# Kernel tuning notes

Hardware: AMD Instinct MI355X
Metric: run time of the kernel (lower is better)

## Reference

```python
import jax, jax.numpy as jnp
import numpy as np
from jax.scipy.special import logsumexp

TAG_NAMES = ['<pad>', 'O', 'B-PER', 'I-PER', 'B-LOC', 'I-LOC', 'B-ORG', 'I-ORG', 'B-MISC', 'I-MISC']
K = len(TAG_NAMES)
T, B, D = 512, 64, 1024
PAD = 0
IMP = -100.0
VOCAB = 30000


def _crf_params(rng):
    # torchcrf reset_parameters: uniform(-0.1, 0.1), then init_crf_transitions overrides
    start = rng.uniform(-0.1, 0.1, K).astype(np.float32)
    end = rng.uniform(-0.1, 0.1, K).astype(np.float32)
    trans = rng.uniform(-0.1, 0.1, (K, K)).astype(np.float32)
    for i, name in enumerate(TAG_NAMES):
        if name[0] in ('I', 'L') or name == '<pad>':
            start[i] = IMP
        if name[0] in ('B', 'I'):
            end[i] = IMP
    tag_is = {p: [i for i, t in enumerate(TAG_NAMES) if t[0] == p] for p in 'BIOUL'}
    tag_is['P'] = [i for i, t in enumerate(TAG_NAMES) if t == 'tag']
    for ft, tos in {'B': 'BOUP', 'I': 'BOUP', 'O': 'IL', 'U': 'IL'}.items():
        for fi in tag_is[ft]:
            for tt in tos:
                for ti in tag_is[tt]:
                    trans[fi, ti] = IMP
    for ft, tos in {'B': 'IL', 'I': 'IL'}.items():
        for fi in tag_is[ft]:
            for tt in tos:
                for ti in tag_is[tt]:
                    if TAG_NAMES[fi].split('-')[1] != TAG_NAMES[ti].split('-')[1]:
                        trans[fi, ti] = IMP
    return jnp.asarray(start), jnp.asarray(end), jnp.asarray(trans)


def setup_inputs() -> dict:
    rng = np.random.default_rng(0)
    # torchcrf requires mask[0] == 1 everywhere and contiguous masks -> build from lengths
    lengths = rng.integers(T // 2, T + 1, size=B)
    valid = np.arange(T)[:, None] < lengths[None, :]  # (T, B)
    words = np.where(valid, rng.integers(1, VOCAB, size=(T, B)), PAD).astype(np.int64)
    tags = rng.integers(0, K, size=(T, B)).astype(np.int64)
    word_features = rng.standard_normal((T, B, D)).astype(np.float32)
    W = (rng.standard_normal((D, K)) / np.sqrt(D)).astype(np.float32)
    b = np.zeros(K, np.float32)
    start, end, trans = _crf_params(rng)
    return dict(words=jnp.asarray(words), tags=jnp.asarray(tags),
                word_features=jnp.asarray(word_features), W=jnp.asarray(W), b=jnp.asarray(b),
                start_trans=start, end_trans=end, transitions=trans)


def _crf_loss(emissions, tags, maskf, start, end, trans):
    """-log p(tags | emissions), summed over batch (torchcrf reduction='sum')."""
    bidx = jnp.arange(emissions.shape[1])
    # gold-path score (numerator)
    score0 = start[tags[0]] + emissions[0, bidx, tags[0]]
    em_tag = jnp.take_along_axis(emissions[1:], tags[1:, :, None], axis=-1)[..., 0]  # (T-1,B)
    step = trans[tags[:-1], tags[1:]] + em_tag
    numer = score0 + jnp.sum(step * maskf[1:], axis=0)
    seq_ends = maskf.sum(0).astype(jnp.int32) - 1
    numer = numer + end[tags[seq_ends, bidx]]
    # partition function (forward algorithm, stable log-sum-exp scan)
    def fwd_step(score, xs):
        em_t, m_t = xs
        nxt = logsumexp(score[:, :, None] + trans[None] + em_t[:, None, :], axis=1)  # (B,K)
        return jnp.where(m_t[:, None] > 0, nxt, score), None
    score, _ = jax.lax.scan(fwd_step, start[None] + emissions[0], (emissions[1:], maskf[1:]))
    denom = logsumexp(score + end[None], axis=1)
    return -(numer - denom).sum()


def _crf_decode(emissions, maskf, start, end, trans):
    """Viterbi decode; returns (T,B) int32 paths, 0-padded past sequence ends."""
    bidx = jnp.arange(emissions.shape[1])
    def vit_step(score, xs):
        em_t, m_t = xs
        bcast = score[:, :, None] + trans[None] + em_t[:, None, :]  # (B, K_prev, K_cur)
        best = bcast.max(axis=1)
        idx = bcast.argmax(axis=1).astype(jnp.int32)
        return jnp.where(m_t[:, None] > 0, best, score), idx
    score, history = jax.lax.scan(vit_step, start[None] + emissions[0], (emissions[1:], maskf[1:]))
    last_tag = jnp.argmax(score + end[None], axis=1).astype(jnp.int32)  # tag at seq_end per batch
    def back_step(tag, xs):
        hist_t, m_t = xs
        prev = jnp.where(m_t > 0, hist_t[bidx, tag], tag)
        return prev, prev
    _, path_head = jax.lax.scan(back_step, last_tag, (history, maskf[1:]), reverse=True)
    paths = jnp.concatenate([path_head, last_tag[None]], axis=0)  # (T, B)
    return jnp.where(maskf > 0, paths, 0)


def reference(words, tags, word_features, W, b, start_trans, end_trans, transitions):
    # eval-mode dropout is identity; fc projects features to tag emissions
    emissions = word_features @ W + b  # (T, B, K)
    maskf = (words != PAD).astype(emissions.dtype)  # (T, B)
    paths = _crf_decode(emissions, maskf, start_trans, end_trans, transitions)
    loss = _crf_loss(emissions, tags, maskf, start_trans, end_trans, transitions)
    return paths, loss
```

## Files before the change

kernel.cpp:

```cpp
#include <hip/hip_runtime.h>
#include <hip/hip_bf16.h>

#define TT 512
#define BB 64
#define KK 10
#define DD 1024
#define CL 32
#define NC 16

typedef unsigned char uchar;
typedef short bf16x8 __attribute__((ext_vector_type(8)));
typedef float f32x4 __attribute__((ext_vector_type(4)));

__device__ __forceinline__ unsigned f2bf(float f) {
    unsigned u = __float_as_uint(f);
    return (u + 0x7FFFu + ((u >> 16) & 1u)) >> 16;
}

__device__ __forceinline__ float max10(const float* r) {
    float m0 = fmaxf(r[0], r[1]), m1 = fmaxf(r[2], r[3]);
    float m2 = fmaxf(r[4], r[5]), m3 = fmaxf(r[6], r[7]);
    float m4 = fmaxf(r[8], r[9]);
    m0 = fmaxf(m0, m1); m2 = fmaxf(m2, m3); m0 = fmaxf(m0, m2);
    return fmaxf(m0, m4);
}

__device__ __forceinline__ float lse10(const float* r) {
    const float m = max10(r);
    float s0 = __expf(r[0] - m) + __expf(r[1] - m);
    float s1 = __expf(r[2] - m) + __expf(r[3] - m);
    float s2 = __expf(r[4] - m) + __expf(r[5] - m);
    float s3 = __expf(r[6] - m) + __expf(r[7] - m);
    float s4 = __expf(r[8] - m) + __expf(r[9] - m);
    return m + __logf(((s0 + s1) + (s2 + s3)) + s4);
}

__global__ __launch_bounds__(512) void k_emissions(
    const int* __restrict__ words, const float* __restrict__ wf,
    const float* __restrict__ W, const float* __restrict__ bias,
    float* __restrict__ em, int* __restrict__ lenArr, float* loss_slot) {
    const int tid = threadIdx.x;
    if (blockIdx.x == 256) {
        __shared__ int cnt[8][64];
        const int b = tid & 63, seg = tid >> 6;
        int c = 0;
        for (int t = seg; t < TT; t += 8) c += (words[t * BB + b] != 0) ? 1 : 0;
        cnt[seg][b] = c;
        __syncthreads();
        if (tid < 64) {
            int s = 0;
            #pragma unroll
            for (int g = 0; g < 8; ++g) s += cnt[g][tid];
            lenArr[tid] = s;
        }
        if (tid == 0) *loss_slot = 0.f;
        return;
    }

    __shared__ uint4 Bfrag[32][64];
    for (int idx = tid; idx < 32 * 64; idx += 512) {
        const int ks = idx >> 6, l = idx & 63;
        const int col = l & 15, kg = l >> 4;
        unsigned u[4];
        #pragma unroll
        for (int p = 0; p < 4; ++p) {
            unsigned lo = 0, hi = 0;
            if (col < KK) {
                const int k0 = ks * 32 + kg * 8 + p * 2;
                lo = f2bf(W[(size_t)k0 * KK + col]);
                hi = f2bf(W[(size_t)(k0 + 1) * KK + col]);
            }
            u[p] = lo | (hi << 16);
        }
        Bfrag[ks][l] = make_uint4(u[0], u[1], u[2], u[3]);
    }
    __syncthreads();

    const int wave = tid >> 6, lane = tid & 63;
    const int arow = lane & 15;
    const int kg   = lane >> 4;
    const int row0 = blockIdx.x * 128 + wave * 16;
    const float* ap = wf + (size_t)(row0 + arow) * DD + kg * 8;
    const float bk = bias[arow < KK ? arow : 0];

    f32x4 acc = {0.f, 0.f, 0.f, 0.f};
    float4 fa[4], fb[4];
    #pragma unroll
    for (int p = 0; p < 4; ++p) {
        fa[p] = *reinterpret_cast<const float4*>(ap + p * 32);
        fb[p] = *reinterpret_cast<const float4*>(ap + p * 32 + 4);
    }
    uint4 bcur[8], bnxt[8];
    #pragma unroll
    for (int q = 0; q < 8; ++q) bcur[q] = Bfrag[q][lane];

    #pragma unroll
    for (int ph = 0; ph < 4; ++ph) {
        if (ph < 3) {
            #pragma unroll
            for (int q = 0; q < 8; ++q) bnxt[q] = Bfrag[(ph + 1) * 8 + q][lane];
        }
        #pragma unroll
        for (int q = 0; q < 8; ++q) {
            const int ks = ph * 8 + q;
            const int s = ks & 3;
            bf16x8 afr;
            afr[0] = (short)f2bf(fa[s].x); afr[1] = (short)f2bf(fa[s].y);
            afr[2] = (short)f2bf(fa[s].z); afr[3] = (short)f2bf(fa[s].w);
            afr[4] = (short)f2bf(fb[s].x); afr[5] = (short)f2bf(fb[s].y);
            afr[6] = (short)f2bf(fb[s].z); afr[7] = (short)f2bf(fb[s].w);
            if (ks < 28) {
                fa[s] = *reinterpret_cast<const float4*>(ap + (ks + 4) * 32);
                fb[s] = *reinterpret_cast<const float4*>(ap + (ks + 4) * 32 + 4);
            }
            union { uint4 u; bf16x8 v; } bu;
            bu.u = bcur[q];
            acc = __builtin_amdgcn_mfma_f32_16x16x32_bf16(afr, bu.v, acc, 0, 0, 0);
        }
        #pragma unroll
        for (int q = 0; q < 8; ++q) bcur[q] = bnxt[q];
    }
    if (arow < KK) {
        #pragma unroll
        for (int r = 0; r < 4; ++r)
            em[(size_t)(row0 + kg * 4 + r) * KK + arow] = acc[r] + bk;
    }
}

__global__ __launch_bounds__(128) void k_chunk(
    const float* __restrict__ em, const float* __restrict__ trans,
    const int* __restrict__ lenArr, float* __restrict__ Mlse, float* __restrict__ Mmax) {
    int id = blockIdx.x;
    const bool mx = id >= 1024; id &= 1023;
    const int b = id >> 4, c = id & 15;
    const int len = lenArr[b];
    const int s_lo = c * CL + 1;
    const int s_hi = min(c * CL + CL, len - 1);
    const int ns = s_hi - s_lo + 1;
    if (ns <= 0) return;

    __shared__ float Ms[KK][12];
    __shared__ float eml[CL][KK];
    const int tid = threadIdx.x;
    for (int idx = tid; idx < CL * KK; idx += 128) {
        const int sl = idx / KK, j = idx % KK;
        const int s = s_lo + sl;
        eml[sl][j] = (s <= TT - 1) ? em[((size_t)s * BB + b) * KK + j] : 0.f;
    }
    const int i = tid / KK, j = tid % KK;
    const bool act = tid < KK * KK;
    float trc[KK];
    if (act) {
        #pragma unroll
        for (int k = 0; k < KK; ++k) trc[k] = trans[k * KK + j];
    }
    __syncthreads();
    float cur = 0.f;
    if (act) { cur = trans[i * KK + j] + eml[0][j]; Ms[i][j] = cur; }
    __syncthreads();
    for (int sl = 1; sl < ns; ++sl) {
        float row[KK];
        if (act) {
            #pragma unroll
            for (int k = 0; k < KK; ++k) row[k] = Ms[i][k] + trc[k];
        }
        __syncthreads();
        if (act) {
            cur = (mx ? max10(row) : lse10(row)) + eml[sl][j];
            Ms[i][j] = cur;
        }
        __syncthreads();
    }
    if (act) {
        float* out = mx ? Mmax : Mlse;
        out[((size_t)b * NC + c) * 100 + i * KK + j] = cur;
    }
}

__global__ __launch_bounds__(1024) void k_crf(
    const int* __restrict__ tags, const float* __restrict__ em,
    const float* __restrict__ startv, const float* __restrict__ endv,
    const float* __restrict__ trans, const int* __restrict__ lenArr,
    const float* __restrict__ Mlse, const float* __restrict__ Mmax,
    int* __restrict__ paths, float* __restrict__ loss_slot) {
    const int b = blockIdx.x;
    const int tid = threadIdx.x;
    const int wv = tid >> 6, lane = tid & 63;
    const int len = lenArr[b];

    __shared__ float Ml[NC][100];
    __shared__ float Mm[NC][100];
    __shared__ float eml[NC][CL][KK];
    __shared__ float ub[NC][KK];
    __shared__ uchar hl[NC][CL * KK];
    __shared__ int   Fl[NC][KK];
    __shared__ int   vt[NC + 1];
    __shared__ float em0[KK];
    __shared__ float red[2];

    for (int idx = tid; idx < NC * 100; idx += 1024) {
        Ml[idx / 100][idx % 100] = Mlse[(size_t)b * NC * 100 + idx];
        Mm[idx / 100][idx % 100] = Mmax[(size_t)b * NC * 100 + idx];
    }
    for (int idx = tid; idx < NC * CL * KK; idx += 1024) {
        const int c = idx / (CL * KK), r = idx % (CL * KK);
        const int sl = r / KK, j = r % KK;
        const int s = c * CL + 1 + sl;
        eml[c][sl][j] = (s <= TT - 1) ? em[((size_t)s * BB + b) * KK + j] : 0.f;
    }
    if (tid < KK) em0[tid] = em[(size_t)b * KK + tid];
    __syncthreads();

    if (wv == 0) {
        float v[KK];
        #pragma unroll
        for (int i = 0; i < KK; ++i) v[i] = startv[i] + em0[i];
        for (int c = 0; c < NC; ++c) {
            if (lane < KK) ub[c][lane] = v[lane];
            const int s_hi = min(c * CL + CL, len - 1);
            if (s_hi >= c * CL + 1) {
                float nv = 0.f;
                if (lane < KK) {
                    float r[KK];
                    #pragma unroll
                    for (int k = 0; k < KK; ++k) r[k] = v[k] + Mm[c][k * KK + lane];
                    nv = max10(r);
                }
                #pragma unroll
                for (int i = 0; i < KK; ++i) v[i] = __shfl(nv, i);
            }
        }
        float best = v[0] + endv[0];
        int bi = 0;
        #pragma unroll
        for (int i = 1; i < KK; ++i) {
            const float x = v[i] + endv[i];
            if (x > best) { best = x; bi = i; }
        }
        if (lane == 0) vt[NC] = bi;
    } else if (wv == 1) {
        float v[KK];
        #pragma unroll
        for (int i = 0; i < KK; ++i) v[i] = startv[i] + em0[i];
        for (int c = 0; c < NC; ++c) {
            const int s_hi = min(c * CL + CL, len - 1);
            if (s_hi >= c * CL + 1) {
                float nv = 0.f;
                if (lane < KK) {
                    float r[KK];
                    #pragma unroll
                    for (int k = 0; k < KK; ++k) r[k] = v[k] + Ml[c][k * KK + lane];
                    nv = lse10(r);
                }
                #pragma unroll
                for (int i = 0; i < KK; ++i) v[i] = __shfl(nv, i);
            }
        }
        float r[KK];
        #pragma unroll
        for (int i = 0; i < KK; ++i) r[i] = v[i] + endv[i];
        if (lane == 0) red[0] = lse10(r);
    } else if (wv == 2) {
        float part = 0.f;
        for (int t = 1 + lane; t < len; t += 64) {
            const int tp = tags[(t - 1) * BB + b];
            const int tc = tags[t * BB + b];
            part += trans[tp * KK + tc] + eml[(t - 1) >> 5][(t - 1) & 31][tc];
        }
        #pragma unroll
        for (int off = 32; off >= 1; off >>= 1) part += __shfl_xor(part, off);
        if (lane == 0) {
            const int t0 = tags[b];
            const int te = tags[(len - 1) * BB + b];
            red[1] = part + startv[t0] + em0[t0] + endv[te];
        }
    }
    __syncthreads();

    {
        const int c = wv;
        const int s_hi = min(c * CL + CL, len - 1);
        const int ns = s_hi - (c * CL + 1) + 1;
        if (ns > 0) {
            float trc[KK];
            if (lane < KK) {
                #pragma unroll
                for (int i = 0; i < KK; ++i) trc[i] = trans[i * KK + lane];
            }
            float s[KK];
            #pragma unroll
            for (int i = 0; i < KK; ++i) s[i] = ub[c][i];
            for (int sl = 0; sl < ns; ++sl) {
                float best = s[0] + trc[0];
                int bi = 0;
                #pragma unroll
                for (int i = 1; i < KK; ++i) {
                    const float x = s[i] + trc[i];
                    if (x > best) { best = x; bi = i; }
                }
                float snew = 0.f;
                if (lane < KK) {
                    snew = best + eml[c][sl][lane];
                    hl[c][sl * KK + lane] = (uchar)bi;
                }
                #pragma unroll
                for (int i = 0; i < KK; ++i) s[i] = __shfl(snew, i);
            }
            if (lane < KK) {
                int cur = lane;
                for (int sl = ns - 1; sl >= 0; --sl) cur = hl[c][sl * KK + cur];
                Fl[c][lane] = cur;
            }
        }
    }
    __syncthreads();

    if (tid == 0) {
        int cur = vt[NC];
        for (int c = NC - 1; c >= 0; --c) {
            const int s_hi = min(c * CL + CL, len - 1);
            if (s_hi >= c * CL + 1) cur = Fl[c][cur];
            vt[c] = cur;
        }
        atomicAdd(loss_slot, red[0] - red[1]);
    }
    __syncthreads();

    const int t0 = wv * CL;
    if (lane < CL) {
        const int t = t0 + lane;
        if (t >= len) paths[t * BB + b] = 0;
    }
    if (lane == 0) {
        const int a = min(t0 + CL, len - 1);
        if (a >= t0) {
            int cur = vt[wv + 1];
            for (int t = a; t >= t0; --t) {
                if (t <= t0 + CL - 1) paths[t * BB + b] = cur;
                if (t > t0) cur = (int)hl[wv][(t - t0 - 1) * KK + cur];
            }
        }
    }
}

extern "C" void kernel_launch(void* const* d_in, const int* in_sizes, int n_in,
                              void* d_out, int out_size, void* d_ws, size_t ws_size,
                              hipStream_t stream) {
    const int*   words  = (const int*)d_in[0];
    const int*   tags   = (const int*)d_in[1];
    const float* wf     = (const float*)d_in[2];
    const float* W      = (const float*)d_in[3];
    const float* bias   = (const float*)d_in[4];
    const float* startv = (const float*)d_in[5];
    const float* endv   = (const float*)d_in[6];
    const float* trans  = (const float*)d_in[7];

    float* em   = (float*)d_ws;
    float* Mlse = em + 327680;
    float* Mmax = Mlse + 102400;
    int*   lenA = (int*)(Mmax + 102400);

    int*   paths     = (int*)d_out;
    float* loss_slot = ((float*)d_out) + TT * BB;

    k_emissions<<<257, 512, 0, stream>>>(words, wf, W, bias, em, lenA, loss_slot);
    k_chunk<<<2048, 128, 0, stream>>>(em, trans, lenA, Mlse, Mmax);
    k_crf<<<64, 1024, 0, stream>>>(tags, em, startv, endv, trans, lenA,
                                   Mlse, Mmax, paths, loss_slot);
}
```

Measured before the change: 78.58 us.

## Stage emission GEMM A-tiles through swizzled double-buffered LDS with coalesced loads

The emission projection kernel now loads word_features with fully coalesced row-strided float4 loads, converts them to bf16 by truncation, and stores them into a double-buffered, XOR-swizzled LDS tile from which each wave reads MFMA A-fragments. Previously each lane read its own row fragment straight from global memory in a strided pattern. The length-count work is folded into block 0 instead of a separate extra block. Truncating instead of rounding to bf16 changes numerics slightly, and the large LDS footprint plus the extra barriers may reduce occupancy.

```diff
diff --git a/kernel.cpp b/kernel.cpp
--- a/kernel.cpp
+++ b/kernel.cpp
@@ -39,9 +39,94 @@
     const int* __restrict__ words, const float* __restrict__ wf,
     const float* __restrict__ W, const float* __restrict__ bias,
     float* __restrict__ em, int* __restrict__ lenArr, float* loss_slot) {
+    __shared__ char  Ab[2][128 * 256];
+    __shared__ uint4 Bfrag[32][64];
+    __shared__ int   cnt[8][64];
+
     const int tid = threadIdx.x;
-    if (blockIdx.x == 256) {
-        __shared__ int cnt[8][64];
+
+    for (int idx = tid; idx < 32 * 64; idx += 512) {
+        const int ks = idx >> 6, l = idx & 63;
+        const int col = l & 15, kg = l >> 4;
+        unsigned u[4];
+        #pragma unroll
+        for (int p = 0; p < 4; ++p) {
+            unsigned lo = 0, hi = 0;
+            if (col < KK) {
+                const int k0 = ks * 32 + kg * 8 + p * 2;
+                lo = f2bf(W[(size_t)k0 * KK + col]);
+                hi = f2bf(W[(size_t)(k0 + 1) * KK + col]);
+            }
+            u[p] = lo | (hi << 16);
+        }
+        Bfrag[ks][l] = make_uint4(u[0], u[1], u[2], u[3]);
+    }
+
+    const int wave = tid >> 6, lane = tid & 63;
+    const int arow = lane & 15;
+    const int kg   = lane >> 4;
+    const int row0blk = blockIdx.x * 128;
+
+    const int srow = tid >> 5;
+    const int scol = (tid & 31) * 4;
+    const float* gbase = wf + (size_t)(row0blk + srow) * DD + scol;
+    const int wr_off = srow * 256 + (((scol >> 3) ^ srow) << 4) + ((scol & 7) * 2);
+
+    float4 st[8];
+    #pragma unroll
+    for (int i = 0; i < 8; ++i) st[i] = *(const float4*)(gbase + i * 16384);
+    #pragma unroll
+    for (int i = 0; i < 8; ++i) {
+        uint2 w;
+        w.x = (__float_as_uint(st[i].x) >> 16) | (__float_as_uint(st[i].y) & 0xFFFF0000u);
+        w.y = (__float_as_uint(st[i].z) >> 16) | (__float_as_uint(st[i].w) & 0xFFFF0000u);
+        *(uint2*)(&Ab[0][wr_off + i * 4096]) = w;
+    }
+    #pragma unroll
+    for (int i = 0; i < 8; ++i) st[i] = *(const float4*)(gbase + 128 + i * 16384);
+    __syncthreads();
+
+    f32x4 acc = {0.f, 0.f, 0.f, 0.f};
+    const int ldsrow = wave * 16 + arow;
+
+    #pragma unroll 1
+    for (int p = 0; p < 8; ++p) {
+        if (p < 7) {
+            if (p > 0) __syncthreads();
+            char* wb = Ab[(p + 1) & 1];
+            #pragma unroll
+            for (int i = 0; i < 8; ++i) {
+                uint2 w;
+                w.x = (__float_as_uint(st[i].x) >> 16) | (__float_as_uint(st[i].y) & 0xFFFF0000u);
+                w.y = (__float_as_uint(st[i].z) >> 16) | (__float_as_uint(st[i].w) & 0xFFFF0000u);
+                *(uint2*)(&wb[wr_off + i * 4096]) = w;
+            }
+            if (p < 6) {
+                const float* gp = gbase + (size_t)(p + 2) * 128;
+                #pragma unroll
+                for (int i = 0; i < 8; ++i) st[i] = *(const float4*)(gp + i * 16384);
+            }
+            __syncthreads();
+        }
+        const char* rb = &Ab[p & 1][ldsrow * 256];
+        #pragma unroll
+        for (int ks = 0; ks < 4; ++ks) {
+            const bf16x8 a = *(const bf16x8*)(rb + (((ks * 4 + kg) ^ arow) << 4));
+            union { uint4 u; bf16x8 v; } bu;
+            bu.u = Bfrag[p * 4 + ks][lane];
+            acc = __builtin_amdgcn_mfma_f32_16x16x32_bf16(a, bu.v, acc, 0, 0, 0);
+        }
+    }
+
+    const int row0 = row0blk + wave * 16;
+    if (arow < KK) {
+        const float bk = bias[arow];
+        #pragma unroll
+        for (int r = 0; r < 4; ++r)
+            em[(size_t)(row0 + kg * 4 + r) * KK + arow] = acc[r] + bk;
+    }
+
+    if (blockIdx.x == 0) {
         const int b = tid & 63, seg = tid >> 6;
         int c = 0;
         for (int t = seg; t < TT; t += 8) c += (words[t * BB + b] != 0) ? 1 : 0;
@@ -54,76 +139,6 @@
             lenArr[tid] = s;
         }
         if (tid == 0) *loss_slot = 0.f;
-        return;
-    }
-
-    __shared__ uint4 Bfrag[32][64];
-    for (int idx = tid; idx < 32 * 64; idx += 512) {
-        const int ks = idx >> 6, l = idx & 63;
-        const int col = l & 15, kg = l >> 4;
-        unsigned u[4];
-        #pragma unroll
-        for (int p = 0; p < 4; ++p) {
-            unsigned lo = 0, hi = 0;
-            if (col < KK) {
-                const int k0 = ks * 32 + kg * 8 + p * 2;
-                lo = f2bf(W[(size_t)k0 * KK + col]);
-                hi = f2bf(W[(size_t)(k0 + 1) * KK + col]);
-            }
-            u[p] = lo | (hi << 16);
-        }
-        Bfrag[ks][l] = make_uint4(u[0], u[1], u[2], u[3]);
-    }
-    __syncthreads();
-
-    const int wave = tid >> 6, lane = tid & 63;
-    const int arow = lane & 15;
-    const int kg   = lane >> 4;
-    const int row0 = blockIdx.x * 128 + wave * 16;
-    const float* ap = wf + (size_t)(row0 + arow) * DD + kg * 8;
-    const float bk = bias[arow < KK ? arow : 0];
-
-    f32x4 acc = {0.f, 0.f, 0.f, 0.f};
-    float4 fa[4], fb[4];
-    #pragma unroll
-    for (int p = 0; p < 4; ++p) {
-        fa[p] = *reinterpret_cast<const float4*>(ap + p * 32);
-        fb[p] = *reinterpret_cast<const float4*>(ap + p * 32 + 4);
-    }
-    uint4 bcur[8], bnxt[8];
-    #pragma unroll
-    for (int q = 0; q < 8; ++q) bcur[q] = Bfrag[q][lane];
-
-    #pragma unroll
-    for (int ph = 0; ph < 4; ++ph) {
-        if (ph < 3) {
-            #pragma unroll
-            for (int q = 0; q < 8; ++q) bnxt[q] = Bfrag[(ph + 1) * 8 + q][lane];
-        }
-        #pragma unroll
-        for (int q = 0; q < 8; ++q) {
-            const int ks = ph * 8 + q;
-            const int s = ks & 3;
-            bf16x8 afr;
-            afr[0] = (short)f2bf(fa[s].x); afr[1] = (short)f2bf(fa[s].y);
-            afr[2] = (short)f2bf(fa[s].z); afr[3] = (short)f2bf(fa[s].w);
-            afr[4] = (short)f2bf(fb[s].x); afr[5] = (short)f2bf(fb[s].y);
-            afr[6] = (short)f2bf(fb[s].z); afr[7] = (short)f2bf(fb[s].w);
-            if (ks < 28) {
-                fa[s] = *reinterpret_cast<const float4*>(ap + (ks + 4) * 32);
-                fb[s] = *reinterpret_cast<const float4*>(ap + (ks + 4) * 32 + 4);
-            }
-            union { uint4 u; bf16x8 v; } bu;
-            bu.u = bcur[q];
-            acc = __builtin_amdgcn_mfma_f32_16x16x32_bf16(afr, bu.v, acc, 0, 0, 0);
-        }
-        #pragma unroll
-        for (int q = 0; q < 8; ++q) bcur[q] = bnxt[q];
-    }
-    if (arow < KK) {
-        #pragma unroll
-        for (int r = 0; r < 4; ++r)
-            em[(size_t)(row0 + kg * 4 + r) * KK + arow] = acc[r] + bk;
     }
 }
 
@@ -363,7 +378,7 @@
     int*   paths     = (int*)d_out;
     float* loss_slot = ((float*)d_out) + TT * BB;
 
-    k_emissions<<<257, 512, 0, stream>>>(words, wf, W, bias, em, lenA, loss_slot);
+    k_emissions<<<256, 512, 0, stream>>>(words, wf, W, bias, em, lenA, loss_slot);
     k_chunk<<<2048, 128, 0, stream>>>(em, trans, lenA, Mlse, Mmax);
     k_crf<<<64, 1024, 0, stream>>>(tags, em, startv, endv, trans, lenA,
                                    Mlse, Mmax, paths, loss_slot);
```

New measurement: 82.75 us. 5.3% more time.

## Split emission GEMM K-dimension across waves with LDS reduction and more blocks

Applied to the files above, without the earlier changes.

The emission projection kernel now launches 2048 small blocks of 256 threads, each computing 16 rows. The four waves each handle a quarter of the 1024-long reduction dimension, and their partial MFMA accumulators are summed through shared memory. The packed W fragment table is compacted to the 10 real columns, with a zero slot standing in for the padding columns. This is meant to spread the memory-bound read of the 128 MB feature tensor over far more blocks and waves to raise bandwidth use. In exchange it adds an LDS reduction, extra barriers, and a per-block rebuild of the W table.

```diff
diff --git a/kernel.cpp b/kernel.cpp
--- a/kernel.cpp
+++ b/kernel.cpp
@@ -35,53 +35,48 @@
     return m + __logf(((s0 + s1) + (s2 + s3)) + s4);
 }
 
-__global__ __launch_bounds__(512) void k_emissions(
+__global__ __launch_bounds__(256, 7) void k_emissions(
     const int* __restrict__ words, const float* __restrict__ wf,
     const float* __restrict__ W, const float* __restrict__ bias,
     float* __restrict__ em, int* __restrict__ lenArr, float* loss_slot) {
+    __shared__ uint4 Bfrag[32 * 40 + 1];
     const int tid = threadIdx.x;
-    if (blockIdx.x == 256) {
-        __shared__ int cnt[8][64];
+
+    if (blockIdx.x == 2048) {
+        int* cnt = (int*)Bfrag;
         const int b = tid & 63, seg = tid >> 6;
         int c = 0;
-        for (int t = seg; t < TT; t += 8) c += (words[t * BB + b] != 0) ? 1 : 0;
-        cnt[seg][b] = c;
+        for (int t = seg; t < TT; t += 4) c += (words[t * BB + b] != 0) ? 1 : 0;
+        cnt[seg * 64 + b] = c;
         __syncthreads();
-        if (tid < 64) {
-            int s = 0;
-            #pragma unroll
-            for (int g = 0; g < 8; ++g) s += cnt[g][tid];
-            lenArr[tid] = s;
-        }
+        if (tid < 64)
+            lenArr[tid] = cnt[tid] + cnt[64 + tid] + cnt[128 + tid] + cnt[192 + tid];
         if (tid == 0) *loss_slot = 0.f;
         return;
     }
 
-    __shared__ uint4 Bfrag[32][64];
-    for (int idx = tid; idx < 32 * 64; idx += 512) {
-        const int ks = idx >> 6, l = idx & 63;
-        const int col = l & 15, kg = l >> 4;
+    for (int idx = tid; idx < 32 * 40; idx += 256) {
+        const int ks = idx / 40, rem = idx - ks * 40;
+        const int kg2 = rem / 10, col = rem - kg2 * 10;
         unsigned u[4];
         #pragma unroll
         for (int p = 0; p < 4; ++p) {
-            unsigned lo = 0, hi = 0;
-            if (col < KK) {
-                const int k0 = ks * 32 + kg * 8 + p * 2;
-                lo = f2bf(W[(size_t)k0 * KK + col]);
-                hi = f2bf(W[(size_t)(k0 + 1) * KK + col]);
-            }
-            u[p] = lo | (hi << 16);
-        }
-        Bfrag[ks][l] = make_uint4(u[0], u[1], u[2], u[3]);
-    }
+            const int k0 = ks * 32 + kg2 * 8 + p * 2;
+            u[p] = f2bf(W[(size_t)k0 * KK + col]) | (f2bf(W[(size_t)(k0 + 1) * KK + col]) << 16);
+        }
+        Bfrag[idx] = make_uint4(u[0], u[1], u[2], u[3]);
+    }
+    if (tid == 0) Bfrag[1280] = make_uint4(0, 0, 0, 0);
     __syncthreads();
 
     const int wave = tid >> 6, lane = tid & 63;
     const int arow = lane & 15;
     const int kg   = lane >> 4;
-    const int row0 = blockIdx.x * 128 + wave * 16;
-    const float* ap = wf + (size_t)(row0 + arow) * DD + kg * 8;
-    const float bk = bias[arow < KK ? arow : 0];
+    const int row0 = blockIdx.x * 16;
+    const float* ap = wf + (size_t)(row0 + arow) * DD + wave * 256 + kg * 8;
+
+    const int bcol  = (arow < KK) ? (wave * 8 * 40 + kg * 10 + arow) : 1280;
+    const int bstep = (arow < KK) ? 40 : 0;
 
     f32x4 acc = {0.f, 0.f, 0.f, 0.f};
     float4 fa[4], fb[4];
@@ -90,40 +85,38 @@
         fa[p] = *reinterpret_cast<const float4*>(ap + p * 32);
         fb[p] = *reinterpret_cast<const float4*>(ap + p * 32 + 4);
     }
-    uint4 bcur[8], bnxt[8];
     #pragma unroll
-    for (int q = 0; q < 8; ++q) bcur[q] = Bfrag[q][lane];
-
-    #pragma unroll
-    for (int ph = 0; ph < 4; ++ph) {
-        if (ph < 3) {
-            #pragma unroll
-            for (int q = 0; q < 8; ++q) bnxt[q] = Bfrag[(ph + 1) * 8 + q][lane];
-        }
-        #pragma unroll
-        for (int q = 0; q < 8; ++q) {
-            const int ks = ph * 8 + q;
-            const int s = ks & 3;
-            bf16x8 afr;
-            afr[0] = (short)f2bf(fa[s].x); afr[1] = (short)f2bf(fa[s].y);
-            afr[2] = (short)f2bf(fa[s].z); afr[3] = (short)f2bf(fa[s].w);
-            afr[4] = (short)f2bf(fb[s].x); afr[5] = (short)f2bf(fb[s].y);
-            afr[6] = (short)f2bf(fb[s].z); afr[7] = (short)f2bf(fb[s].w);
-            if (ks < 28) {
-                fa[s] = *reinterpret_cast<const float4*>(ap + (ks + 4) * 32);
-                fb[s] = *reinterpret_cast<const float4*>(ap + (ks + 4) * 32 + 4);
-            }
-            union { uint4 u; bf16x8 v; } bu;
-            bu.u = bcur[q];
-            acc = __builtin_amdgcn_mfma_f32_16x16x32_bf16(afr, bu.v, acc, 0, 0, 0);
-        }
-        #pragma unroll
-        for (int q = 0; q < 8; ++q) bcur[q] = bnxt[q];
-    }
-    if (arow < KK) {
+    for (int s = 0; s < 8; ++s) {
+        const int r = s & 3;
+        bf16x8 afr;
+        afr[0] = (short)f2bf(fa[r].x); afr[1] = (short)f2bf(fa[r].y);
+        afr[2] = (short)f2bf(fa[r].z); afr[3] = (short)f2bf(fa[r].w);
+        afr[4] = (short)f2bf(fb[r].x); afr[5] = (short)f2bf(fb[r].y);
+        afr[6] = (short)f2bf(fb[r].z); afr[7] = (short)f2bf(fb[r].w);
+        if (s < 4) {
+            fa[r] = *reinterpret_cast<const float4*>(ap + (s + 4) * 32);
+            fb[r] = *reinterpret_cast<const float4*>(ap + (s + 4) * 32 + 4);
+        }
+        union { uint4 u; bf16x8 v; } bu;
+        bu.u = Bfrag[bcol + s * bstep];
+        acc = __builtin_amdgcn_mfma_f32_16x16x32_bf16(afr, bu.v, acc, 0, 0, 0);
+    }
+
+    __syncthreads();
+    f32x4* red = (f32x4*)Bfrag;
+    red[wave * 64 + lane] = acc;
+    __syncthreads();
+    if (wave == 0 && arow < KK) {
+        f32x4 sum = red[lane];
+        #pragma unroll
+        for (int w = 1; w < 4; ++w) {
+            const f32x4 t = red[w * 64 + lane];
+            sum[0] += t[0]; sum[1] += t[1]; sum[2] += t[2]; sum[3] += t[3];
+        }
+        const float bk = bias[arow];
         #pragma unroll
         for (int r = 0; r < 4; ++r)
-            em[(size_t)(row0 + kg * 4 + r) * KK + arow] = acc[r] + bk;
+            em[(size_t)(row0 + kg * 4 + r) * KK + arow] = sum[r] + bk;
     }
 }
 
@@ -363,7 +356,7 @@
     int*   paths     = (int*)d_out;
     float* loss_slot = ((float*)d_out) + TT * BB;
 
-    k_emissions<<<257, 512, 0, stream>>>(words, wf, W, bias, em, lenA, loss_slot);
+    k_emissions<<<2049, 256, 0, stream>>>(words, wf, W, bias, em, lenA, loss_slot);
     k_chunk<<<2048, 128, 0, stream>>>(em, trans, lenA, Mlse, Mmax);
     k_crf<<<64, 1024, 0, stream>>>(tags, em, startv, endv, trans, lenA,
                                    Mlse, Mmax, paths, loss_slot);
```

New measurement: 97.52 us. +24.1%, slower.

## Stream emission GEMM A-tiles through LDS via async global_load_lds double buffering

Applied to the files above, without the earlier changes.

Replaces the per-lane register float4 prefetch of word_features in the emissions GEMM with asynchronous global-to-LDS loads (global_load_lds, 16 bytes per lane) into a double-buffered, XOR-swizzled per-wave LDS slab. Each iteration waits on vmcnt, reads two K-slices from LDS, issues the next prefetch, and runs two bf16 MFMAs. The aim is deeper memory-level parallelism and fewer VGPRs on this bandwidth-bound 128 MB read. In exchange it uses 64 KB of extra LDS per block, which may limit occupancy, and adds LDS round-trips and hand-placed waitcnt ordering.

```diff
diff --git a/kernel.cpp b/kernel.cpp
--- a/kernel.cpp
+++ b/kernel.cpp
@@ -7,6 +7,9 @@
 #define DD 1024
 #define CL 32
 #define NC 16
+
+#define AS1 __attribute__((address_space(1)))
+#define AS3 __attribute__((address_space(3)))
 
 typedef unsigned char uchar;
 typedef short bf16x8 __attribute__((ext_vector_type(8)));
@@ -39,34 +42,36 @@
     const int* __restrict__ words, const float* __restrict__ wf,
     const float* __restrict__ W, const float* __restrict__ bias,
     float* __restrict__ em, int* __restrict__ lenArr, float* loss_slot) {
+    __shared__ char  Ab[2][8][4096];
+    __shared__ uint4 Bfrag[32][64];
+
     const int tid = threadIdx.x;
     if (blockIdx.x == 256) {
-        __shared__ int cnt[8][64];
+        int* cnt = (int*)&Ab[0][0][0];
         const int b = tid & 63, seg = tid >> 6;
         int c = 0;
         for (int t = seg; t < TT; t += 8) c += (words[t * BB + b] != 0) ? 1 : 0;
-        cnt[seg][b] = c;
+        cnt[seg * 64 + b] = c;
         __syncthreads();
         if (tid < 64) {
             int s = 0;
             #pragma unroll
-            for (int g = 0; g < 8; ++g) s += cnt[g][tid];
+            for (int g = 0; g < 8; ++g) s += cnt[g * 64 + tid];
             lenArr[tid] = s;
         }
         if (tid == 0) *loss_slot = 0.f;
         return;
     }
 
-    __shared__ uint4 Bfrag[32][64];
     for (int idx = tid; idx < 32 * 64; idx += 512) {
         const int ks = idx >> 6, l = idx & 63;
-        const int col = l & 15, kg = l >> 4;
+        const int col = l & 15, kg2 = l >> 4;
         unsigned u[4];
         #pragma unroll
         for (int p = 0; p < 4; ++p) {
             unsigned lo = 0, hi = 0;
             if (col < KK) {
-                const int k0 = ks * 32 + kg * 8 + p * 2;
+                const int k0 = ks * 32 + kg2 * 8 + p * 2;
                 lo = f2bf(W[(size_t)k0 * KK + col]);
                 hi = f2bf(W[(size_t)(k0 + 1) * KK + col]);
             }
@@ -80,46 +85,74 @@
     const int arow = lane & 15;
     const int kg   = lane >> 4;
     const int row0 = blockIdx.x * 128 + wave * 16;
-    const float* ap = wf + (size_t)(row0 + arow) * DD + kg * 8;
     const float bk = bias[arow < KK ? arow : 0];
 
+    const int rr = lane >> 4;
+    const int cc = lane & 15;
+    const float* gsrc[4];
+    #pragma unroll
+    for (int i = 0; i < 4; ++i) {
+        const int rloc = i * 4 + rr;
+        gsrc[i] = wf + (size_t)(row0 + rloc) * DD + (cc ^ (rloc & 7)) * 4;
+    }
+
+#define ISSUE(P, B) do { \
+    _Pragma("unroll") \
+    for (int i_ = 0; i_ < 4; ++i_) { \
+        __builtin_amdgcn_global_load_lds( \
+            (const AS1 unsigned int*)(gsrc[i_] + (P) * 64), \
+            (AS3 unsigned int*)&Ab[B][wave][i_ * 1024], 16, 0, 0); \
+    } \
+} while (0)
+
+    ISSUE(0, 0);
+    ISSUE(1, 1);
+
     f32x4 acc = {0.f, 0.f, 0.f, 0.f};
-    float4 fa[4], fb[4];
-    #pragma unroll
-    for (int p = 0; p < 4; ++p) {
-        fa[p] = *reinterpret_cast<const float4*>(ap + p * 32);
-        fb[p] = *reinterpret_cast<const float4*>(ap + p * 32 + 4);
-    }
-    uint4 bcur[8], bnxt[8];
-    #pragma unroll
-    for (int q = 0; q < 8; ++q) bcur[q] = Bfrag[q][lane];
-
-    #pragma unroll
-    for (int ph = 0; ph < 4; ++ph) {
-        if (ph < 3) {
-            #pragma unroll
-            for (int q = 0; q < 8; ++q) bnxt[q] = Bfrag[(ph + 1) * 8 + q][lane];
-        }
-        #pragma unroll
-        for (int q = 0; q < 8; ++q) {
-            const int ks = ph * 8 + q;
-            const int s = ks & 3;
-            bf16x8 afr;
-            afr[0] = (short)f2bf(fa[s].x); afr[1] = (short)f2bf(fa[s].y);
-            afr[2] = (short)f2bf(fa[s].z); afr[3] = (short)f2bf(fa[s].w);
-            afr[4] = (short)f2bf(fb[s].x); afr[5] = (short)f2bf(fb[s].y);
-            afr[6] = (short)f2bf(fb[s].z); afr[7] = (short)f2bf(fb[s].w);
-            if (ks < 28) {
-                fa[s] = *reinterpret_cast<const float4*>(ap + (ks + 4) * 32);
-                fb[s] = *reinterpret_cast<const float4*>(ap + (ks + 4) * 32 + 4);
-            }
-            union { uint4 u; bf16x8 v; } bu;
-            bu.u = bcur[q];
-            acc = __builtin_amdgcn_mfma_f32_16x16x32_bf16(afr, bu.v, acc, 0, 0, 0);
-        }
-        #pragma unroll
-        for (int q = 0; q < 8; ++q) bcur[q] = bnxt[q];
-    }
+    const int sw = arow & 7;
+    const char* slab = &Ab[0][wave][0];
+    const int rbase = arow * 256;
+
+    #pragma unroll 1
+    for (int p = 0; p < 16; ++p) {
+        const int b = p & 1;
+        if (p < 15) { asm volatile("s_waitcnt vmcnt(4)" ::: "memory"); }
+        else        { asm volatile("s_waitcnt vmcnt(0)" ::: "memory"); }
+        __builtin_amdgcn_sched_barrier(0);
+
+        const char* rb = slab + b * 32768 + rbase;
+        f32x4 fa0, fb0, fa1, fb1;
+        uint4 B0, B1;
+        {
+            fa0 = *(const f32x4*)(rb + (((kg * 2)     ^ sw) << 4));
+            fb0 = *(const f32x4*)(rb + (((kg * 2 + 1) ^ sw) << 4));
+            B0 = Bfrag[p * 2][lane];
+        }
+        {
+            fa1 = *(const f32x4*)(rb + (((8 + kg * 2)     ^ sw) << 4));
+            fb1 = *(const f32x4*)(rb + (((8 + kg * 2 + 1) ^ sw) << 4));
+            B1 = Bfrag[p * 2 + 1][lane];
+        }
+        asm volatile("s_waitcnt lgkmcnt(0)" ::: "memory");
+        __builtin_amdgcn_sched_barrier(0);
+        if (p < 14) ISSUE(p + 2, b);
+
+        bf16x8 a0, a1;
+        a0[0] = (short)f2bf(fa0[0]); a0[1] = (short)f2bf(fa0[1]);
+        a0[2] = (short)f2bf(fa0[2]); a0[3] = (short)f2bf(fa0[3]);
+        a0[4] = (short)f2bf(fb0[0]); a0[5] = (short)f2bf(fb0[1]);
+        a0[6] = (short)f2bf(fb0[2]); a0[7] = (short)f2bf(fb0[3]);
+        a1[0] = (short)f2bf(fa1[0]); a1[1] = (short)f2bf(fa1[1]);
+        a1[2] = (short)f2bf(fa1[2]); a1[3] = (short)f2bf(fa1[3]);
+        a1[4] = (short)f2bf(fb1[0]); a1[5] = (short)f2bf(fb1[1]);
+        a1[6] = (short)f2bf(fb1[2]); a1[7] = (short)f2bf(fb1[3]);
+        union { uint4 u; bf16x8 v; } bu0, bu1;
+        bu0.u = B0; bu1.u = B1;
+        acc = __builtin_amdgcn_mfma_f32_16x16x32_bf16(a0, bu0.v, acc, 0, 0, 0);
+        acc = __builtin_amdgcn_mfma_f32_16x16x32_bf16(a1, bu1.v, acc, 0, 0, 0);
+    }
+#undef ISSUE
+
     if (arow < KK) {
         #pragma unroll
         for (int r = 0; r < 4; ++r)
```

New measurement: 84.10 us. 1.07x slower.
